# Performance work log

Hardware: AMD Instinct MI355X
Metric: run time of the kernel (lower is better)

## Reference

```python
import jax, jax.numpy as jnp
import numpy as np

N, E, G = 8192, 65536, 16          # atoms, edges, graphs in batch
NUM_ELEM, C, NB = 10, 64, 8        # elements, hidden channels, bessel basis
LMAX, NLAYERS = 3, 2
LM = (LMAX + 1) ** 2               # 16 spherical-harmonic components
R_MAX, P_CUT = 5.0, 5
EPS = 1e-9


def spherical_harmonics(u):
    # u: [E,3] unit vectors -> real spherical harmonics l<=3, [E,16]
    x, y, z = u[:, 0], u[:, 1], u[:, 2]
    x2, y2, z2 = x * x, y * y, z * z
    sh = [
        jnp.full_like(x, 0.28209479177387814),
        0.4886025119029199 * y, 0.4886025119029199 * z, 0.4886025119029199 * x,
        1.0925484305920792 * x * y, 1.0925484305920792 * y * z,
        0.31539156525252005 * (3.0 * z2 - 1.0),
        1.0925484305920792 * x * z, 0.5462742152960396 * (x2 - y2),
        0.5900435899266435 * y * (3.0 * x2 - y2), 2.890611442640554 * x * y * z,
        0.4570457994644658 * y * (5.0 * z2 - 1.0),
        0.3731763325901154 * z * (5.0 * z2 - 3.0),
        0.4570457994644658 * x * (5.0 * z2 - 1.0),
        1.445305721320277 * z * (x2 - y2),
        0.5900435899266435 * x * (x2 - 3.0 * y2),
    ]
    return jnp.stack(sh, axis=-1)


def radial_embedding(r):
    # Bessel radial basis with polynomial envelope cutoff -> [E, NB]
    u = r / R_MAX
    p = float(P_CUT)
    cut = (1.0 - 0.5 * (p + 1.0) * (p + 2.0) * u ** P_CUT
           + p * (p + 2.0) * u ** (P_CUT + 1)
           - 0.5 * p * (p + 1.0) * u ** (P_CUT + 2))
    cut = jnp.where(u < 1.0, cut, 0.0)
    n = jnp.arange(1, NB + 1, dtype=r.dtype)
    bessel = jnp.sqrt(2.0 / R_MAX) * jnp.sin(n[None, :] * jnp.pi * u[:, None]) \
             / jnp.maximum(r, EPS)[:, None]
    return bessel * cut[:, None]


def setup_inputs() -> dict:
    key = jax.random.key(0)
    ks = jax.random.split(key, 10)
    positions = jax.random.uniform(ks[0], (N, 3), jnp.float32) * 10.0
    elems = jax.random.randint(ks[1], (N,), 0, NUM_ELEM)
    node_attrs = jax.nn.one_hot(elems, NUM_ELEM, dtype=jnp.float32)
    edge_index = jax.random.randint(ks[2], (2, E), 0, N).astype(jnp.int32)
    shifts = jnp.zeros((E, 3), jnp.float32)
    batch = jnp.sort(jax.random.randint(ks[3], (N,), 0, G)).astype(jnp.int32)
    W_embed = jax.random.normal(ks[4], (NUM_ELEM, C), jnp.float32) / np.sqrt(NUM_ELEM)
    atomic_energies_w = jnp.arange(-1.0, -(NUM_ELEM + 1.0), -1.0, dtype=jnp.float32)
    W_rad = jax.random.normal(ks[5], (NLAYERS, NB, C), jnp.float32) / np.sqrt(NB)
    W_prod = jax.random.normal(ks[6], (NLAYERS, NUM_ELEM, (LMAX + 1) * C, C),
                               jnp.float32) / np.sqrt((LMAX + 1) * C)
    w_read = jax.random.normal(ks[7], (C,), jnp.float32) / np.sqrt(C)
    return {"positions": positions, "node_attrs": node_attrs, "shifts": shifts,
            "W_embed": W_embed, "atomic_energies_w": atomic_energies_w,
            "W_rad": W_rad, "W_prod": W_prod, "w_read": w_read,
            "edge_index": edge_index, "batch": batch}


def _energy(positions, node_attrs, shifts, W_embed, atomic_energies_w,
            W_rad, W_prod, w_read, edge_index, batch):
    snd, rcv = edge_index[0], edge_index[1]
    vec = positions[rcv] - positions[snd] + shifts            # [E,3]
    length = jnp.sqrt(jnp.sum(vec * vec, axis=-1) + EPS)      # [E]
    Y = spherical_harmonics(vec / length[:, None])            # [E,LM]
    R = radial_embedding(length)                              # [E,NB]

    e0 = jax.ops.segment_sum(node_attrs @ atomic_energies_w, batch, num_segments=G)
    h = node_attrs @ W_embed                                  # [N,C]

    for layer in range(NLAYERS):
        w = R @ W_rad[layer]                                  # [E,C] radial weights
        msg = (w * h[snd])[:, None, :] * Y[:, :, None]        # [E,LM,C] tensor product
        A = jax.ops.segment_sum(msg, rcv, num_segments=N)     # [N,LM,C] atomic basis
        A2 = A * A
        # invariant (rotation-invariant) contraction: sum over m within each l
        B = jnp.concatenate(
            [A2[:, l * l:(l + 1) * (l + 1), :].sum(axis=1) for l in range(LMAX + 1)],
            axis=-1)                                          # [N,(LMAX+1)*C]
        # element-dependent product-basis mixing
        h = jnp.einsum('nf,efc,ne->nc', B, W_prod[layer], node_attrs)

    node_e = h @ w_read                                       # [N]
    inter_e = jax.ops.segment_sum(node_e, batch, num_segments=G)
    return e0 + inter_e                                       # [G]


def reference(positions, node_attrs, shifts, W_embed, atomic_energies_w,
              W_rad, W_prod, w_read, edge_index, batch):
    energy = _energy(positions, node_attrs, shifts, W_embed, atomic_energies_w,
                     W_rad, W_prod, w_read, edge_index, batch)
    forces = -jax.grad(
        lambda p: _energy(p, node_attrs, shifts, W_embed, atomic_energies_w,
                          W_rad, W_prod, w_read, edge_index, batch).sum()
    )(positions)
    return energy, forces
```

## Files before the change

### kernel.cpp

```cpp
#include <hip/hip_runtime.h>
#include <math.h>

#define NN 8192
#define NE 65536
#define NG 16
#define NEL 10
#define CC 64
#define NLM 16
#define MAXST 16
#define PI_F 3.14159265358979f

__device__ __forceinline__ int lm_l(int lm) {
    return (lm == 0) ? 0 : (lm < 4) ? 1 : (lm < 9) ? 2 : 3;
}

__device__ __forceinline__ void stage_pack(
    const float* __restrict__ PK, const int* __restrict__ SSND,
    int beg, int cnt, int c, float* sPK, int* sS)
{
    int tot = cnt * 24;
    for (int i = c; i < tot; i += 64) sPK[i] = PK[(size_t)beg*24 + i];
    if (c < cnt) sS[c] = SSND[beg + c];
    __builtin_amdgcn_wave_barrier();
}

__global__ __launch_bounds__(256) void k_front(
    const float* __restrict__ pos, const float* __restrict__ shifts,
    const int* __restrict__ snd, const int* __restrict__ rcv,
    float* __restrict__ Y, float* __restrict__ R,
    float* __restrict__ U, float* __restrict__ L, int* __restrict__ cnt,
    const float* __restrict__ attrs, const float* __restrict__ Wemb,
    const float* __restrict__ aew, const int* __restrict__ batch,
    float* __restrict__ h0, int* __restrict__ elem, int* __restrict__ ecnt,
    float* __restrict__ out,
    const float* __restrict__ Wprod1, const float* __restrict__ wread,
    float* __restrict__ vb1)
{
    __shared__ int hcnt[NEL];
    int bx = blockIdx.x;
    if (bx < 256) {
        int e = bx * 256 + threadIdx.x;
        int s = snd[e], r = rcv[e];
        float vx = pos[r*3+0] - pos[s*3+0] + shifts[e*3+0];
        float vy = pos[r*3+1] - pos[s*3+1] + shifts[e*3+1];
        float vz = pos[r*3+2] - pos[s*3+2] + shifts[e*3+2];
        float len = sqrtf(vx*vx + vy*vy + vz*vz + 1e-9f);
        L[e] = len;
        if (len >= 5.0f) return;
        atomicAdd(&cnt[r], 1);
        float x = vx/len, y = vy/len, z = vz/len;
        U[e*3+0] = x; U[e*3+1] = y; U[e*3+2] = z;
        float x2 = x*x, y2 = y*y, z2 = z*z;
        float4* Yv = (float4*)(Y + (size_t)e*16);
        Yv[0] = make_float4(0.28209479177387814f,
                            0.4886025119029199f*y,
                            0.4886025119029199f*z,
                            0.4886025119029199f*x);
        Yv[1] = make_float4(1.0925484305920792f*x*y,
                            1.0925484305920792f*y*z,
                            0.31539156525252005f*(3.f*z2 - 1.f),
                            1.0925484305920792f*x*z);
        Yv[2] = make_float4(0.5462742152960396f*(x2 - y2),
                            0.5900435899266435f*y*(3.f*x2 - y2),
                            2.890611442640554f*x*y*z,
                            0.4570457994644658f*y*(5.f*z2 - 1.f));
        Yv[3] = make_float4(0.3731763325901154f*z*(5.f*z2 - 3.f),
                            0.4570457994644658f*x*(5.f*z2 - 1.f),
                            1.445305721320277f*z*(x2 - y2),
                            0.5900435899266435f*x*(x2 - 3.f*y2));
        float ur = len * 0.2f;
        float u2 = ur*ur, u4 = u2*u2, u5 = u4*ur, u6 = u5*ur, u7 = u6*ur;
        float cut = 1.f - 21.f*u5 + 35.f*u6 - 15.f*u7;
        const float s2f = 0.632455532033676f;
        float th = (PI_F/5.f) * len;
        float s1, c1; sincosf(th, &s1, &c1);
        float sn_ = s1, cs = c1;
        float coef = s2f * cut / len;
        float rv[8];
#pragma unroll
        for (int nb = 0; nb < 8; nb++) {
            rv[nb] = coef * sn_;
            float ns = sn_*c1 + cs*s1;
            float nc = cs*c1 - sn_*s1;
            sn_ = ns; cs = nc;
        }
        float4* Rv = (float4*)(R + (size_t)e*8);
        Rv[0] = make_float4(rv[0], rv[1], rv[2], rv[3]);
        Rv[1] = make_float4(rv[4], rv[5], rv[6], rv[7]);
    } else if (bx < 768) {
        int t = threadIdx.x, c = t & 63, w = t >> 6;
        if (t < NEL) hcnt[t] = 0;
        __syncthreads();
        float esum = 0.f; int curb = -1;
        for (int g = 0; g < 4; g++) {
            int n = (bx - 256)*16 + w*4 + g;
            float hv = 0.f;
            for (int el = 0; el < NEL; el++) hv += attrs[n*NEL+el] * Wemb[el*CC+c];
            h0[(size_t)n*CC+c] = hv;
            int el = 0; float e0 = 0.f;
            for (int k = 0; k < NEL; k++) {
                float a = attrs[n*NEL+k];
                e0 += a * aew[k];
                if (a > 0.5f) el = k;
            }
            if (c == 0) {
                elem[n] = el;
                atomicAdd(&hcnt[el], 1);
            }
            int b = batch[n];
            if (b != curb) {
                if (curb >= 0 && c == 0) atomicAdd(&out[curb], esum);
                curb = b; esum = 0.f;
            }
            esum += e0;
        }
        if (curb >= 0 && c == 0) atomicAdd(&out[curb], esum);
        __syncthreads();
        if (t < NEL) { int v = hcnt[t]; if (v) atomicAdd(&ecnt[t], v); }
    } else {
        int el = bx - 768, f = threadIdx.x;
        float s = 0.f;
        for (int c = 0; c < CC; c++) s += wread[c] * Wprod1[(size_t)el*256*CC + f*CC + c];
        vb1[el*256+f] = s;
    }
}

__global__ __launch_bounds__(1024) void k_scan(
    const int* __restrict__ cnt, int* __restrict__ offs,
    const int* __restrict__ ecnt, int* __restrict__ eoff)
{
    __shared__ int wsum[16];
    int t = threadIdx.x, lane = t & 63, w = t >> 6;
    int loc[8];
    int run = 0;
#pragma unroll
    for (int i = 0; i < 8; i++) { int v = cnt[t*8+i]; loc[i] = run; run += v; }
    int v = run;
#pragma unroll
    for (int o = 1; o < 64; o <<= 1) {
        int u = __shfl_up(v, o, 64);
        if (lane >= o) v += u;
    }
    if (lane == 63) wsum[w] = v;
    __syncthreads();
    if (t < 16) {
        int x = wsum[t];
#pragma unroll
        for (int o = 1; o < 16; o <<= 1) {
            int u = __shfl_up(x, o, 64);
            if (t >= o) x += u;
        }
        wsum[t] = x;
    }
    __syncthreads();
    int wpre = (w == 0) ? 0 : wsum[w-1];
    int pre = wpre + v - run;
#pragma unroll
    for (int i = 0; i < 8; i++) offs[t*8+i] = pre + loc[i];
    if (t == 1023) offs[NN] = pre + run;
    if (t == 0) {
        int r = 0;
        for (int el = 0; el < NEL; el++) { eoff[el] = r; r += ecnt[el]; }
        eoff[NEL] = r;
    }
}

__global__ void k_scatpack(
    const int* __restrict__ snd, const int* __restrict__ rcv,
    const float* __restrict__ Y, const float* __restrict__ R,
    const float* __restrict__ U, const float* __restrict__ L,
    const int* __restrict__ offs, int* __restrict__ cur,
    float* __restrict__ PK, int* __restrict__ SSND, int* __restrict__ SRCV,
    float* __restrict__ UL,
    const int* __restrict__ elem, const int* __restrict__ eoff,
    int* __restrict__ ecur, int* __restrict__ nbe)
{
    int e = blockIdx.x * blockDim.x + threadIdx.x;
    if (e < NN) {
        int el = elem[e];
        int p = eoff[el] + atomicAdd(&ecur[el], 1);
        nbe[p] = e;
    }
    if (e >= NE) return;
    if (L[e] >= 5.0f) return;
    int r = rcv[e];
    int p = offs[r] + atomicAdd(&cur[r], 1);
    const float4* Yp = (const float4*)(Y + (size_t)e*16);
    float4* d = (float4*)(PK + (size_t)p*24);
    d[0] = Yp[0]; d[1] = Yp[1]; d[2] = Yp[2]; d[3] = Yp[3];
    const float4* Rp = (const float4*)(R + (size_t)e*8);
    d[4] = Rp[0]; d[5] = Rp[1];
    SSND[p] = snd[e];
    SRCV[p] = rcv[e];
    ((float4*)UL)[p] = make_float4(U[e*3+0], U[e*3+1], U[e*3+2], L[e]);
}

__global__ __launch_bounds__(256) void k_fwd0(
    const float* __restrict__ PK, const int* __restrict__ SSND,
    const float* __restrict__ Wrad0, const float* __restrict__ Wprod0,
    const float* __restrict__ h0, const float* __restrict__ attrs,
    const int* __restrict__ elem, const int* __restrict__ offs,
    const int* __restrict__ nbe, float* __restrict__ h1)
{
    __shared__ __align__(16) float sB[4][512];
    __shared__ __align__(16) float sPK[4][MAXST*24];
    __shared__ int sS[4][MAXST];
    int t = threadIdx.x, c = t & 63, w = t >> 6;
    float wr[8];
#pragma unroll
    for (int nb = 0; nb < 8; nb++) wr[nb] = Wrad0[nb*CC+c];
    int nid[2], nel[2]; float na[2];
#pragma unroll
    for (int g = 0; g < 2; g++) {
        int n = nbe[blockIdx.x*8 + w*2 + g];
        nid[g] = n;
        int el = elem[n]; nel[g] = el; na[g] = attrs[n*NEL+el];
        float acc[NLM];
#pragma unroll
        for (int lm = 0; lm < NLM; lm++) acc[lm] = 0.f;
        int beg = offs[n], end = offs[n+1];
        for (int base = beg; base < end; base += MAXST) {
            int m = min(MAXST, end - base);
            stage_pack(PK, SSND, base, m, c, sPK[w], sS[w]);
            for (int cb = 0; cb < m; cb += 4) {
                float hb[4];
#pragma unroll
                for (int k = 0; k < 4; k++)
                    hb[k] = (cb+k < m) ? h0[(size_t)sS[w][cb+k]*CC + c] : 0.f;
#pragma unroll
                for (int jj = 0; jj < 4; jj++) {
                    if (cb+jj >= m) break;
                    const float* rec = &sPK[w][(cb+jj)*24];
                    float wv = 0.f;
#pragma unroll
                    for (int nb = 0; nb < 8; nb++) wv += rec[16+nb]*wr[nb];
                    float tt = wv * hb[jj];
#pragma unroll
                    for (int lm = 0; lm < NLM; lm++) acc[lm] += rec[lm]*tt;
                }
            }
            __builtin_amdgcn_wave_barrier();
        }
        float b0 = acc[0]*acc[0];
        float b1 = acc[1]*acc[1] + acc[2]*acc[2] + acc[3]*acc[3];
        float b2 = acc[4]*acc[4] + acc[5]*acc[5] + acc[6]*acc[6] + acc[7]*acc[7] + acc[8]*acc[8];
        float b3 = 0.f;
#pragma unroll
        for (int lm = 9; lm < 16; lm++) b3 += acc[lm]*acc[lm];
        sB[w][g*256 + 0*64 + c] = b0;
        sB[w][g*256 + 1*64 + c] = b1;
        sB[w][g*256 + 2*64 + c] = b2;
        sB[w][g*256 + 3*64 + c] = b3;
    }
    __builtin_amdgcn_wave_barrier();
    float hv[2] = {0.f, 0.f};
    int done = 0;
    while (done != 0x3) {
        int g0 = __ffs(~done & 0x3) - 1;
        int el = g0 ? nel[1] : nel[0];
        int msk = 0;
#pragma unroll
        for (int g = 0; g < 2; g++) if (nel[g] == el) msk |= 1 << g;
        const float* Wn = Wprod0 + (size_t)el*256*CC;
        float tmp[2] = {0.f, 0.f};
        for (int f4 = 0; f4 < 64; f4++) {
            float wv0 = Wn[(f4*4+0)*CC + c];
            float wv1 = Wn[(f4*4+1)*CC + c];
            float wv2 = Wn[(f4*4+2)*CC + c];
            float wv3 = Wn[(f4*4+3)*CC + c];
#pragma unroll
            for (int g = 0; g < 2; g++) {
                float4 b = *((const float4*)&sB[w][g*256 + f4*4]);
                tmp[g] += b.x*wv0 + b.y*wv1 + b.z*wv2 + b.w*wv3;
            }
        }
#pragma unroll
        for (int g = 0; g < 2; g++) if ((msk >> g) & 1) hv[g] = tmp[g];
        done |= msk;
    }
#pragma unroll
    for (int g = 0; g < 2; g++) h1[(size_t)nid[g]*CC + c] = na[g]*hv[g];
}

__global__ __launch_bounds__(256) void k_gseed(
    const float* __restrict__ gh1, const float* __restrict__ Wprod0,
    const float* __restrict__ attrs, const int* __restrict__ elem,
    const int* __restrict__ nbe, float* __restrict__ GB)
{
    __shared__ __align__(16) float sgh[4][2][64];
    int t = threadIdx.x, c = t & 63, w = t >> 6;
    int nid[2], nel[2]; float na[2];
#pragma unroll
    for (int g = 0; g < 2; g++) {
        int n = nbe[blockIdx.x*8 + w*2 + g];
        nid[g] = n;
        int el = elem[n]; nel[g] = el; na[g] = attrs[n*NEL+el];
        sgh[w][g][c] = gh1[(size_t)n*CC + c];
    }
    __builtin_amdgcn_wave_barrier();
    float outv[4][2];
    int done = 0;
    while (done != 0x3) {
        int g0 = __ffs(~done & 0x3) - 1;
        int el = g0 ? nel[1] : nel[0];
        int msk = 0;
#pragma unroll
        for (int g = 0; g < 2; g++) if (nel[g] == el) msk |= 1 << g;
        const float* W0 = Wprod0 + (size_t)el*256*CC;
#pragma unroll
        for (int l = 0; l < 4; l++) {
            const float4* row = (const float4*)(W0 + (size_t)(l*64 + c)*CC);
            float t2[2] = {0.f, 0.f};
#pragma unroll 4
            for (int k4 = 0; k4 < 16; k4++) {
                float4 wv = row[k4];
#pragma unroll
                for (int g = 0; g < 2; g++) {
                    float4 gg = *((const float4*)&sgh[w][g][k4*4]);
                    t2[g] += wv.x*gg.x + wv.y*gg.y + wv.z*gg.z + wv.w*gg.w;
                }
            }
#pragma unroll
            for (int g = 0; g < 2; g++) if ((msk >> g) & 1) outv[l][g] = t2[g];
        }
        done |= msk;
    }
#pragma unroll
    for (int g = 0; g < 2; g++)
#pragma unroll
        for (int l = 0; l < 4; l++)
            GB[(size_t)nid[g]*256 + l*64 + c] = na[g]*outv[l][g];
}

__global__ __launch_bounds__(256) void k_fbwd(
    const float* __restrict__ PK, const int* __restrict__ SSND,
    const float* __restrict__ Wrad, const float* __restrict__ hprev,
    const float* __restrict__ vb1, const float* __restrict__ GB,
    const float* __restrict__ attrs, const int* __restrict__ elem,
    const int* __restrict__ batch, const int* __restrict__ offs,
    float* __restrict__ gYp, float* __restrict__ gRp, float* __restrict__ gh,
    float* __restrict__ out, int layer1)
{
    __shared__ __align__(16) float wrls[8*68];
    __shared__ __align__(16) float sPK[4][MAXST*24];
    __shared__ int sS[4][MAXST];
    __shared__ __align__(16) float Mls[4][16*68];
    __shared__ __align__(16) float Tls[4][4*68];
    __shared__ __align__(16) float Gls[4][4*68];
    int t = threadIdx.x, c = t & 63, w = t >> 6;
    float wr[8];
#pragma unroll
    for (int nb = 0; nb < 8; nb++) wr[nb] = Wrad[nb*CC+c];
    if (w == 0) {
#pragma unroll
        for (int nb = 0; nb < 8; nb++) wrls[nb*68+c] = wr[nb];
    }
    __syncthreads();
    float esum = 0.f; int curb = -1;
    for (int g = 0; g < 2; g++) {
        int n = blockIdx.x*8 + w*2 + g;
        int el = elem[n];
        float a = attrs[n*NEL+el];
        float g4[4];
        if (layer1) {
#pragma unroll
            for (int l = 0; l < 4; l++) g4[l] = a * vb1[el*256 + l*64 + c];
        } else {
#pragma unroll
            for (int l = 0; l < 4; l++) g4[l] = GB[(size_t)n*256 + l*64 + c];
        }
        int beg = offs[n], end = offs[n+1];
        int cnt = end - beg;
        float acc[NLM];
#pragma unroll
        for (int lm = 0; lm < NLM; lm++) acc[lm] = 0.f;
        for (int base = beg; base < end; base += MAXST) {
            int m = min(MAXST, end - base);
            stage_pack(PK, SSND, base, m, c, sPK[w], sS[w]);
            for (int cb = 0; cb < m; cb += 4) {
                float hb[4];
#pragma unroll
                for (int k = 0; k < 4; k++)
                    hb[k] = (cb+k < m) ? hprev[(size_t)sS[w][cb+k]*CC + c] : 0.f;
#pragma unroll
                for (int jj = 0; jj < 4; jj++) {
                    if (cb+jj >= m) break;
                    const float* rec = &sPK[w][(cb+jj)*24];
                    float wv = 0.f;
#pragma unroll
                    for (int nb = 0; nb < 8; nb++) wv += rec[16+nb]*wr[nb];
                    float tt = wv * hb[jj];
#pragma unroll
                    for (int lm = 0; lm < NLM; lm++) acc[lm] += rec[lm]*tt;
                }
            }
            __builtin_amdgcn_wave_barrier();
        }
        if (layer1) {
            float b0 = acc[0]*acc[0];
            float b1 = acc[1]*acc[1] + acc[2]*acc[2] + acc[3]*acc[3];
            float b2 = acc[4]*acc[4] + acc[5]*acc[5] + acc[6]*acc[6] + acc[7]*acc[7] + acc[8]*acc[8];
            float b3 = 0.f;
#pragma unroll
            for (int lm = 9; lm < 16; lm++) b3 += acc[lm]*acc[lm];
            float ep = b0*vb1[el*256+c] + b1*vb1[el*256+64+c]
                     + b2*vb1[el*256+128+c] + b3*vb1[el*256+192+c];
#pragma unroll
            for (int o = 32; o > 0; o >>= 1) ep += __shfl_xor(ep, o, 64);
            int b = batch[n];
            if (b != curb) {
                if (curb >= 0 && c == 0) atomicAdd(&out[curb], esum);
                curb = b; esum = 0.f;
            }
            esum += a * ep;
        }
        float M[NLM];
#pragma unroll
        for (int lm = 0; lm < NLM; lm++) {
            M[lm] = 2.f * acc[lm] * g4[lm_l(lm)];
            Mls[w][lm*68+c] = M[lm];
        }
        __builtin_amdgcn_wave_barrier();
        bool cached = (cnt <= MAXST);
        for (int base = beg; base < end; base += MAXST) {
            int m = min(MAXST, end - base);
            if (!cached) stage_pack(PK, SSND, base, m, c, sPK[w], sS[w]);
            for (int cb = 0; cb < m; cb += 4) {
                int ncq = min(4, m - cb);
                float hb[4];
#pragma unroll
                for (int k = 0; k < 4; k++)
                    hb[k] = (cb+k < m) ? hprev[(size_t)sS[w][cb+k]*CC + c] : 0.f;
#pragma unroll
                for (int jj = 0; jj < 4; jj++) {
                    if (jj >= ncq) break;
                    const float* rec = &sPK[w][(cb+jj)*24];
                    float wv = 0.f;
#pragma unroll
                    for (int nb = 0; nb < 8; nb++) wv += rec[16+nb]*wr[nb];
                    float hvv = hb[jj];
                    float my = 0.f;
#pragma unroll
                    for (int lm = 0; lm < NLM; lm++) my += M[lm]*rec[lm];
                    Tls[w][jj*68+c] = wv * hvv;
                    Gls[w][jj*68+c] = hvv * my;
                    if (layer1) atomicAdd(&gh[(size_t)sS[w][cb+jj]*CC + c], wv * my);
                }
                __builtin_amdgcn_wave_barrier();
                {
                    int jj = c >> 4, lm = c & 15;
                    if (jj < ncq) {
                        const float4* mrow = (const float4*)&Mls[w][lm*68];
                        const float4* trow = (const float4*)&Tls[w][jj*68];
                        float s_ = 0.f;
#pragma unroll
                        for (int k4 = 0; k4 < 16; k4++) {
                            float4 mm = mrow[k4]; float4 tv = trow[k4];
                            s_ += mm.x*tv.x + mm.y*tv.y + mm.z*tv.z + mm.w*tv.w;
                        }
                        size_t p = (size_t)(base + cb + jj);
                        if (layer1) gYp[p*16+lm] = s_;
                        else        gYp[p*16+lm] += s_;
                    }
                }
                if (c < 32) {
                    int jj = c >> 3, nb = c & 7;
                    if (jj < ncq) {
                        const float4* wrow = (const float4*)&wrls[nb*68];
                        const float4* grow = (const float4*)&Gls[w][jj*68];
                        float s_ = 0.f;
#pragma unroll
                        for (int k4 = 0; k4 < 16; k4++) {
                            float4 wv4 = wrow[k4]; float4 gv = grow[k4];
                            s_ += wv4.x*gv.x + wv4.y*gv.y + wv4.z*gv.z + wv4.w*gv.w;
                        }
                        size_t p = (size_t)(base + cb + jj);
                        if (layer1) gRp[p*8+nb] = s_;
                        else        gRp[p*8+nb] += s_;
                    }
                }
                __builtin_amdgcn_wave_barrier();
            }
        }
    }
    if (curb >= 0 && c == 0) atomicAdd(&out[curb], esum);
}

__global__ void k_geo_bwd(const float* __restrict__ gYp, const float* __restrict__ gRp,
                          const float* __restrict__ UL, const int* __restrict__ SSND,
                          const int* __restrict__ SRCV, const int* __restrict__ offs,
                          float* __restrict__ F)
{
    int p = blockIdx.x * blockDim.x + threadIdx.x;
    if (p >= offs[NN]) return;
    float4 ul = ((const float4*)UL)[p];
    float x = ul.x, y = ul.y, z = ul.z, len = ul.w;
    float g[16];
    {
        const float4* gv = (const float4*)(gYp + (size_t)p*16);
        float4 a0 = gv[0], a1 = gv[1], a2 = gv[2], a3 = gv[3];
        g[0]=a0.x; g[1]=a0.y; g[2]=a0.z; g[3]=a0.w;
        g[4]=a1.x; g[5]=a1.y; g[6]=a1.z; g[7]=a1.w;
        g[8]=a2.x; g[9]=a2.y; g[10]=a2.z; g[11]=a2.w;
        g[12]=a3.x; g[13]=a3.y; g[14]=a3.z; g[15]=a3.w;
    }
    float gr[8];
    {
        const float4* rv = (const float4*)(gRp + (size_t)p*8);
        float4 r0 = rv[0], r1 = rv[1];
        gr[0]=r0.x; gr[1]=r0.y; gr[2]=r0.z; gr[3]=r0.w;
        gr[4]=r1.x; gr[5]=r1.y; gr[6]=r1.z; gr[7]=r1.w;
    }
    float x2 = x*x, y2 = y*y, z2 = z*z;
    float gx = 0.f, gy = 0.f, gz = 0.f;
    gx += 0.4886025119029199f*g[3];
    gy += 0.4886025119029199f*g[1];
    gz += 0.4886025119029199f*g[2];
    gx += 1.0925484305920792f*y*g[4];  gy += 1.0925484305920792f*x*g[4];
    gy += 1.0925484305920792f*z*g[5];  gz += 1.0925484305920792f*y*g[5];
    gz += 1.8923493915151203f*z*g[6];
    gx += 1.0925484305920792f*z*g[7];  gz += 1.0925484305920792f*x*g[7];
    gx += 1.0925484305920792f*x*g[8];  gy -= 1.0925484305920792f*y*g[8];
    gx += 3.540261539559861f*x*y*g[9];
    gy += 0.5900435899266435f*(3.f*x2 - 3.f*y2)*g[9];
    gx += 2.890611442640554f*y*z*g[10]; gy += 2.890611442640554f*x*z*g[10]; gz += 2.890611442640554f*x*y*g[10];
    gy += 0.4570457994644658f*(5.f*z2 - 1.f)*g[11]; gz += 4.570457994644658f*y*z*g[11];
    gz += 0.3731763325901154f*(15.f*z2 - 3.f)*g[12];
    gx += 0.4570457994644658f*(5.f*z2 - 1.f)*g[13]; gz += 4.570457994644658f*x*z*g[13];
    gx += 2.890611442640554f*x*z*g[14]; gy -= 2.890611442640554f*y*z*g[14];
    gz += 1.445305721320277f*(x2 - y2)*g[14];
    gx += 0.5900435899266435f*(3.f*x2 - 3.f*y2)*g[15];
    gy -= 3.540261539559861f*x*y*g[15];
    float ur = len * 0.2f;
    float gL = 0.f;
    {
        float u2 = ur*ur, u4 = u2*u2, u5 = u4*ur, u6 = u5*ur, u7 = u6*ur;
        float poly  = 1.f - 21.f*u5 + 35.f*u6 - 15.f*u7;
        float dpoly = (-105.f*u4 + 210.f*u5 - 105.f*u6)*0.2f;
        const float s2f = 0.632455532033676f;
        const float k1 = PI_F/5.f;
        float th = k1*len;
        float s1, c1; sincosf(th, &s1, &c1);
        float sn_ = s1, cs = c1;
        float inv_r = 1.f/len;
        bool tiny = (len < 2e-3f);
#pragma unroll
        for (int nb = 0; nb < 8; nb++) {
            float kn = k1*(float)(nb+1);
            float bes = s2f*sn_*inv_r;
            float dbes;
            if (tiny) dbes = -s2f*kn*kn*kn*len*(1.f/3.f);
            else      dbes = s2f*(kn*cs - sn_*inv_r)*inv_r;
            gL += gr[nb]*(dbes*poly + bes*dpoly);
            float ns = sn_*c1 + cs*s1;
            float nc = cs*c1 - sn_*s1;
            sn_ = ns; cs = nc;
        }
    }
    float dot = gx*x + gy*y + gz*z;
    float gvx = (gx - dot*x)/len + gL*x;
    float gvy = (gy - dot*y)/len + gL*y;
    float gvz = (gz - dot*z)/len + gL*z;
    int sn = SSND[p], rn = SRCV[p];
    atomicAdd(&F[rn*3+0], -gvx);
    atomicAdd(&F[rn*3+1], -gvy);
    atomicAdd(&F[rn*3+2], -gvz);
    atomicAdd(&F[sn*3+0],  gvx);
    atomicAdd(&F[sn*3+1],  gvy);
    atomicAdd(&F[sn*3+2],  gvz);
}

extern "C" void kernel_launch(void* const* d_in, const int* in_sizes, int n_in,
                              void* d_out, int out_size, void* d_ws, size_t ws_size,
                              hipStream_t stream)
{
    const float* positions  = (const float*)d_in[0];
    const float* node_attrs = (const float*)d_in[1];
    const float* shifts     = (const float*)d_in[2];
    const float* W_embed    = (const float*)d_in[3];
    const float* aew        = (const float*)d_in[4];
    const float* W_rad      = (const float*)d_in[5];
    const float* W_prod     = (const float*)d_in[6];
    const float* w_read     = (const float*)d_in[7];
    const int*   edge_index = (const int*)d_in[8];
    const int*   batch      = (const int*)d_in[9];
    float* out = (float*)d_out;

    const int* snd = edge_index;
    const int* rcv = edge_index + NE;

    char* ws = (char*)d_ws;
    size_t off = 0;
    auto allocf = [&](size_t nelems) -> float* {
        float* p = (float*)(ws + off); off += nelems * sizeof(float); return p;
    };
    float* Y    = allocf((size_t)NE*16);
    float* R    = allocf((size_t)NE*8);
    float* U    = allocf((size_t)NE*3);
    float* L    = allocf((size_t)NE);
    float* PK   = allocf((size_t)NE*24);
    float* UL   = allocf((size_t)NE*4);
    float* H0   = allocf((size_t)NN*CC);
    float* H1   = allocf((size_t)NN*CC);
    float* GYP  = allocf((size_t)NE*16);
    float* GRP  = allocf((size_t)NE*8);
    float* GB   = allocf((size_t)NN*256);
    float* VB1  = allocf((size_t)NEL*256);
    size_t zero_off = off;
    float* GH1  = allocf((size_t)NN*CC);
    int* CNT   = (int*)(ws + off); off += (size_t)NN*4;
    int* CUR   = (int*)(ws + off); off += (size_t)NN*4;
    int* ECNT  = (int*)(ws + off); off += 16*4;
    int* ECUR  = (int*)(ws + off); off += 16*4;
    size_t zero_bytes = off - zero_off;
    int* ELEM  = (int*)(ws + off); off += (size_t)NN*4;
    int* OFFS  = (int*)(ws + off); off += (size_t)(NN+1)*4;
    int* SSND  = (int*)(ws + off); off += (size_t)NE*4;
    int* SRCV  = (int*)(ws + off); off += (size_t)NE*4;
    int* ELOFF = (int*)(ws + off); off += 16*4;
    int* NBE   = (int*)(ws + off); off += (size_t)NN*4;

    hipMemsetAsync(out, 0, (size_t)out_size * sizeof(float), stream);
    hipMemsetAsync(ws + zero_off, 0, zero_bytes, stream);

    const float* Wrad0  = W_rad;
    const float* Wrad1  = W_rad + 8*CC;
    const float* Wprod0 = W_prod;
    const float* Wprod1 = W_prod + (size_t)NEL*256*CC;

    k_front<<<256 + 512 + NEL, 256, 0, stream>>>(
        positions, shifts, snd, rcv, Y, R, U, L, CNT,
        node_attrs, W_embed, aew, batch, H0, ELEM, ECNT, out,
        Wprod1, w_read, VB1);
    k_scan<<<1, 1024, 0, stream>>>(CNT, OFFS, ECNT, ELOFF);
    k_scatpack<<<NE/256, 256, 0, stream>>>(snd, rcv, Y, R, U, L, OFFS, CUR,
                                           PK, SSND, SRCV, UL, ELEM, ELOFF, ECUR, NBE);

    k_fwd0<<<NN/8, 256, 0, stream>>>(PK, SSND, Wrad0, Wprod0, H0, node_attrs, ELEM,
                                     OFFS, NBE, H1);
    k_fbwd<<<NN/8, 256, 0, stream>>>(PK, SSND, Wrad1, H1, VB1, GB, node_attrs, ELEM,
                                     batch, OFFS, GYP, GRP, GH1, out, 1);
    k_gseed<<<NN/8, 256, 0, stream>>>(GH1, Wprod0, node_attrs, ELEM, NBE, GB);
    k_fbwd<<<NN/8, 256, 0, stream>>>(PK, SSND, Wrad0, H0, VB1, GB, node_attrs, ELEM,
                                     batch, OFFS, GYP, GRP, GH1, out, 0);

    k_geo_bwd<<<NE/256, 256, 0, stream>>>(GYP, GRP, UL, SSND, SRCV, OFFS, out + NG);
    (void)in_sizes; (void)n_in; (void)ws_size;
}
```

Before: 285.2 us.

## Cache layer-0 atomic basis from forward pass and process four nodes per wave

The forward layer-0 kernel now writes the per-node A coefficients to a workspace buffer. The layer-0 backward pass reads them back instead of recomputing the edge gather and sum. The staging size doubles to 32 edges, and each wave handles four nodes instead of two, which halves the grid and amortizes the Wprod weight loads across more nodes. The cost is an extra 32 MB write and read of A0, plus more shared memory and registers per block, which may reduce occupancy.

```diff
diff --git a/kernel.cpp b/kernel.cpp
--- a/kernel.cpp
+++ b/kernel.cpp
@@ -7,7 +7,7 @@
 #define NEL 10
 #define CC 64
 #define NLM 16
-#define MAXST 16
+#define MAXST 32
 #define PI_F 3.14159265358979f
 
 __device__ __forceinline__ int lm_l(int lm) {
@@ -200,19 +200,20 @@
     const float* __restrict__ Wrad0, const float* __restrict__ Wprod0,
     const float* __restrict__ h0, const float* __restrict__ attrs,
     const int* __restrict__ elem, const int* __restrict__ offs,
-    const int* __restrict__ nbe, float* __restrict__ h1)
-{
-    __shared__ __align__(16) float sB[4][512];
+    const int* __restrict__ nbe, float* __restrict__ h1,
+    float* __restrict__ A0)
+{
+    __shared__ __align__(16) float sB[4][1024];
     __shared__ __align__(16) float sPK[4][MAXST*24];
     __shared__ int sS[4][MAXST];
     int t = threadIdx.x, c = t & 63, w = t >> 6;
     float wr[8];
 #pragma unroll
     for (int nb = 0; nb < 8; nb++) wr[nb] = Wrad0[nb*CC+c];
-    int nid[2], nel[2]; float na[2];
-#pragma unroll
-    for (int g = 0; g < 2; g++) {
-        int n = nbe[blockIdx.x*8 + w*2 + g];
+    int nid[4], nel[4]; float na[4];
+#pragma unroll
+    for (int g = 0; g < 4; g++) {
+        int n = nbe[blockIdx.x*16 + w*4 + g];
         nid[g] = n;
         int el = elem[n]; nel[g] = el; na[g] = attrs[n*NEL+el];
         float acc[NLM];
@@ -241,6 +242,8 @@
             }
             __builtin_amdgcn_wave_barrier();
         }
+#pragma unroll
+        for (int lm = 0; lm < NLM; lm++) A0[(size_t)n*1024 + lm*64 + c] = acc[lm];
         float b0 = acc[0]*acc[0];
         float b1 = acc[1]*acc[1] + acc[2]*acc[2] + acc[3]*acc[3];
         float b2 = acc[4]*acc[4] + acc[5]*acc[5] + acc[6]*acc[6] + acc[7]*acc[7] + acc[8]*acc[8];
@@ -253,33 +256,33 @@
         sB[w][g*256 + 3*64 + c] = b3;
     }
     __builtin_amdgcn_wave_barrier();
-    float hv[2] = {0.f, 0.f};
+    float hv[4] = {0.f, 0.f, 0.f, 0.f};
     int done = 0;
-    while (done != 0x3) {
-        int g0 = __ffs(~done & 0x3) - 1;
-        int el = g0 ? nel[1] : nel[0];
+    while (done != 0xF) {
+        int g0 = __ffs(~done & 0xF) - 1;
+        int el = (g0==0) ? nel[0] : (g0==1) ? nel[1] : (g0==2) ? nel[2] : nel[3];
         int msk = 0;
 #pragma unroll
-        for (int g = 0; g < 2; g++) if (nel[g] == el) msk |= 1 << g;
+        for (int g = 0; g < 4; g++) if (nel[g] == el) msk |= 1 << g;
         const float* Wn = Wprod0 + (size_t)el*256*CC;
-        float tmp[2] = {0.f, 0.f};
+        float tmp[4] = {0.f, 0.f, 0.f, 0.f};
         for (int f4 = 0; f4 < 64; f4++) {
             float wv0 = Wn[(f4*4+0)*CC + c];
             float wv1 = Wn[(f4*4+1)*CC + c];
             float wv2 = Wn[(f4*4+2)*CC + c];
             float wv3 = Wn[(f4*4+3)*CC + c];
 #pragma unroll
-            for (int g = 0; g < 2; g++) {
+            for (int g = 0; g < 4; g++) {
                 float4 b = *((const float4*)&sB[w][g*256 + f4*4]);
                 tmp[g] += b.x*wv0 + b.y*wv1 + b.z*wv2 + b.w*wv3;
             }
         }
 #pragma unroll
-        for (int g = 0; g < 2; g++) if ((msk >> g) & 1) hv[g] = tmp[g];
+        for (int g = 0; g < 4; g++) if ((msk >> g) & 1) hv[g] = tmp[g];
         done |= msk;
     }
 #pragma unroll
-    for (int g = 0; g < 2; g++) h1[(size_t)nid[g]*CC + c] = na[g]*hv[g];
+    for (int g = 0; g < 4; g++) h1[(size_t)nid[g]*CC + c] = na[g]*hv[g];
 }
 
 __global__ __launch_bounds__(256) void k_gseed(
@@ -287,46 +290,46 @@
     const float* __restrict__ attrs, const int* __restrict__ elem,
     const int* __restrict__ nbe, float* __restrict__ GB)
 {
-    __shared__ __align__(16) float sgh[4][2][64];
+    __shared__ __align__(16) float sgh[4][4][64];
     int t = threadIdx.x, c = t & 63, w = t >> 6;
-    int nid[2], nel[2]; float na[2];
-#pragma unroll
-    for (int g = 0; g < 2; g++) {
-        int n = nbe[blockIdx.x*8 + w*2 + g];
+    int nid[4], nel[4]; float na[4];
+#pragma unroll
+    for (int g = 0; g < 4; g++) {
+        int n = nbe[blockIdx.x*16 + w*4 + g];
         nid[g] = n;
         int el = elem[n]; nel[g] = el; na[g] = attrs[n*NEL+el];
         sgh[w][g][c] = gh1[(size_t)n*CC + c];
     }
     __builtin_amdgcn_wave_barrier();
-    float outv[4][2];
+    float outv[4][4];
     int done = 0;
-    while (done != 0x3) {
-        int g0 = __ffs(~done & 0x3) - 1;
-        int el = g0 ? nel[1] : nel[0];
+    while (done != 0xF) {
+        int g0 = __ffs(~done & 0xF) - 1;
+        int el = (g0==0) ? nel[0] : (g0==1) ? nel[1] : (g0==2) ? nel[2] : nel[3];
         int msk = 0;
 #pragma unroll
-        for (int g = 0; g < 2; g++) if (nel[g] == el) msk |= 1 << g;
+        for (int g = 0; g < 4; g++) if (nel[g] == el) msk |= 1 << g;
         const float* W0 = Wprod0 + (size_t)el*256*CC;
 #pragma unroll
         for (int l = 0; l < 4; l++) {
             const float4* row = (const float4*)(W0 + (size_t)(l*64 + c)*CC);
-            float t2[2] = {0.f, 0.f};
+            float t4[4] = {0.f, 0.f, 0.f, 0.f};
 #pragma unroll 4
             for (int k4 = 0; k4 < 16; k4++) {
                 float4 wv = row[k4];
 #pragma unroll
-                for (int g = 0; g < 2; g++) {
+                for (int g = 0; g < 4; g++) {
                     float4 gg = *((const float4*)&sgh[w][g][k4*4]);
-                    t2[g] += wv.x*gg.x + wv.y*gg.y + wv.z*gg.z + wv.w*gg.w;
+                    t4[g] += wv.x*gg.x + wv.y*gg.y + wv.z*gg.z + wv.w*gg.w;
                 }
             }
 #pragma unroll
-            for (int g = 0; g < 2; g++) if ((msk >> g) & 1) outv[l][g] = t2[g];
+            for (int g = 0; g < 4; g++) if ((msk >> g) & 1) outv[l][g] = t4[g];
         }
         done |= msk;
     }
 #pragma unroll
-    for (int g = 0; g < 2; g++)
+    for (int g = 0; g < 4; g++)
 #pragma unroll
         for (int l = 0; l < 4; l++)
             GB[(size_t)nid[g]*256 + l*64 + c] = na[g]*outv[l][g];
@@ -336,6 +339,7 @@
     const float* __restrict__ PK, const int* __restrict__ SSND,
     const float* __restrict__ Wrad, const float* __restrict__ hprev,
     const float* __restrict__ vb1, const float* __restrict__ GB,
+    const float* __restrict__ A0,
     const float* __restrict__ attrs, const int* __restrict__ elem,
     const int* __restrict__ batch, const int* __restrict__ offs,
     float* __restrict__ gYp, float* __restrict__ gRp, float* __restrict__ gh,
@@ -357,8 +361,8 @@
     }
     __syncthreads();
     float esum = 0.f; int curb = -1;
-    for (int g = 0; g < 2; g++) {
-        int n = blockIdx.x*8 + w*2 + g;
+    for (int g = 0; g < 4; g++) {
+        int n = blockIdx.x*16 + w*4 + g;
         int el = elem[n];
         float a = attrs[n*NEL+el];
         float g4[4];
@@ -372,31 +376,33 @@
         int beg = offs[n], end = offs[n+1];
         int cnt = end - beg;
         float acc[NLM];
-#pragma unroll
-        for (int lm = 0; lm < NLM; lm++) acc[lm] = 0.f;
-        for (int base = beg; base < end; base += MAXST) {
-            int m = min(MAXST, end - base);
-            stage_pack(PK, SSND, base, m, c, sPK[w], sS[w]);
-            for (int cb = 0; cb < m; cb += 4) {
-                float hb[4];
-#pragma unroll
-                for (int k = 0; k < 4; k++)
-                    hb[k] = (cb+k < m) ? hprev[(size_t)sS[w][cb+k]*CC + c] : 0.f;
-#pragma unroll
-                for (int jj = 0; jj < 4; jj++) {
-                    if (cb+jj >= m) break;
-                    const float* rec = &sPK[w][(cb+jj)*24];
-                    float wv = 0.f;
-#pragma unroll
-                    for (int nb = 0; nb < 8; nb++) wv += rec[16+nb]*wr[nb];
-                    float tt = wv * hb[jj];
-#pragma unroll
-                    for (int lm = 0; lm < NLM; lm++) acc[lm] += rec[lm]*tt;
+        bool cached = false;
+        if (layer1) {
+#pragma unroll
+            for (int lm = 0; lm < NLM; lm++) acc[lm] = 0.f;
+            for (int base = beg; base < end; base += MAXST) {
+                int m = min(MAXST, end - base);
+                stage_pack(PK, SSND, base, m, c, sPK[w], sS[w]);
+                for (int cb = 0; cb < m; cb += 4) {
+                    float hb[4];
+#pragma unroll
+                    for (int k = 0; k < 4; k++)
+                        hb[k] = (cb+k < m) ? hprev[(size_t)sS[w][cb+k]*CC + c] : 0.f;
+#pragma unroll
+                    for (int jj = 0; jj < 4; jj++) {
+                        if (cb+jj >= m) break;
+                        const float* rec = &sPK[w][(cb+jj)*24];
+                        float wv = 0.f;
+#pragma unroll
+                        for (int nb = 0; nb < 8; nb++) wv += rec[16+nb]*wr[nb];
+                        float tt = wv * hb[jj];
+#pragma unroll
+                        for (int lm = 0; lm < NLM; lm++) acc[lm] += rec[lm]*tt;
+                    }
                 }
-            }
-            __builtin_amdgcn_wave_barrier();
-        }
-        if (layer1) {
+                __builtin_amdgcn_wave_barrier();
+            }
+            cached = (cnt <= MAXST);
             float b0 = acc[0]*acc[0];
             float b1 = acc[1]*acc[1] + acc[2]*acc[2] + acc[3]*acc[3];
             float b2 = acc[4]*acc[4] + acc[5]*acc[5] + acc[6]*acc[6] + acc[7]*acc[7] + acc[8]*acc[8];
@@ -413,6 +419,9 @@
                 curb = b; esum = 0.f;
             }
             esum += a * ep;
+        } else {
+#pragma unroll
+            for (int lm = 0; lm < NLM; lm++) acc[lm] = A0[(size_t)n*1024 + lm*64 + c];
         }
         float M[NLM];
 #pragma unroll
@@ -421,7 +430,6 @@
             Mls[w][lm*68+c] = M[lm];
         }
         __builtin_amdgcn_wave_barrier();
-        bool cached = (cnt <= MAXST);
         for (int base = beg; base < end; base += MAXST) {
             int m = min(MAXST, end - base);
             if (!cached) stage_pack(PK, SSND, base, m, c, sPK[w], sS[w]);
@@ -602,6 +610,7 @@
     float* UL   = allocf((size_t)NE*4);
     float* H0   = allocf((size_t)NN*CC);
     float* H1   = allocf((size_t)NN*CC);
+    float* A0   = allocf((size_t)NN*1024);
     float* GYP  = allocf((size_t)NE*16);
     float* GRP  = allocf((size_t)NE*8);
     float* GB   = allocf((size_t)NN*256);
@@ -636,13 +645,13 @@
     k_scatpack<<<NE/256, 256, 0, stream>>>(snd, rcv, Y, R, U, L, OFFS, CUR,
                                            PK, SSND, SRCV, UL, ELEM, ELOFF, ECUR, NBE);
 
-    k_fwd0<<<NN/8, 256, 0, stream>>>(PK, SSND, Wrad0, Wprod0, H0, node_attrs, ELEM,
-                                     OFFS, NBE, H1);
-    k_fbwd<<<NN/8, 256, 0, stream>>>(PK, SSND, Wrad1, H1, VB1, GB, node_attrs, ELEM,
-                                     batch, OFFS, GYP, GRP, GH1, out, 1);
-    k_gseed<<<NN/8, 256, 0, stream>>>(GH1, Wprod0, node_attrs, ELEM, NBE, GB);
-    k_fbwd<<<NN/8, 256, 0, stream>>>(PK, SSND, Wrad0, H0, VB1, GB, node_attrs, ELEM,
-                                     batch, OFFS, GYP, GRP, GH1, out, 0);
+    k_fwd0<<<NN/16, 256, 0, stream>>>(PK, SSND, Wrad0, Wprod0, H0, node_attrs, ELEM,
+                                      OFFS, NBE, H1, A0);
+    k_fbwd<<<NN/16, 256, 0, stream>>>(PK, SSND, Wrad1, H1, VB1, GB, A0, node_attrs, ELEM,
+                                      batch, OFFS, GYP, GRP, GH1, out, 1);
+    k_gseed<<<NN/16, 256, 0, stream>>>(GH1, Wprod0, node_attrs, ELEM, NBE, GB);
+    k_fbwd<<<NN/16, 256, 0, stream>>>(PK, SSND, Wrad0, H0, VB1, GB, A0, node_attrs, ELEM,
+                                      batch, OFFS, GYP, GRP, GH1, out, 0);
 
     k_geo_bwd<<<NE/256, 256, 0, stream>>>(GYP, GRP, UL, SSND, SRCV, OFFS, out + NG);
     (void)in_sizes; (void)n_in; (void)ws_size;
```

After: 288.1 us. About the same (+1.0%).
